# Kernel tuning notes

Hardware: AMD Instinct MI355X
Metric: run time of the kernel (lower is better)

Reference implementation:

```python
import jax, jax.numpy as jnp
import numpy as np

B, T, S = 8, 2048, 512          # batch, visual (tgt) len, audio (src) len
VD, AD, E, H = 512, 256, 512, 8 # v_dim, a_dim, embed_dim, num_heads
D = E // H                      # head_dim = 64
CLAMP = 50000.0


def _xavier(key, fan_in, fan_out):
    limit = float(np.sqrt(6.0 / (fan_in + fan_out)))
    return jax.random.uniform(key, (fan_in, fan_out), jnp.float32, -limit, limit)


def setup_inputs() -> dict:
    key = jax.random.key(0)
    ks = jax.random.split(key, 8)
    return {
        "v": jax.random.normal(ks[0], (B, T, VD), jnp.float32),
        "a": jax.random.normal(ks[1], (B, S, AD), jnp.float32),
        # weights stored [in, out]; biases zero per _reset_parameters
        "w_vq": _xavier(ks[2], VD, E), "b_vq": jnp.zeros((E,), jnp.float32),
        "w_ak": _xavier(ks[3], AD, E), "b_ak": jnp.zeros((E,), jnp.float32),
        "w_vv": _xavier(ks[4], VD, E), "b_vv": jnp.zeros((E,), jnp.float32),
        "w_av": _xavier(ks[5], AD, E), "b_av": jnp.zeros((E,), jnp.float32),
        "w_ov": _xavier(ks[6], E, VD), "b_ov": jnp.zeros((VD,), jnp.float32),
        "w_oa": _xavier(ks[7], E, AD), "b_oa": jnp.zeros((AD,), jnp.float32),
    }


def _heads(x):
    # [B, L, E] -> [B, L, H, D]
    return x.reshape(x.shape[0], x.shape[1], H, D)


def reference(v, a, w_vq, b_vq, w_ak, b_ak, w_vv, b_vv, w_av, b_av,
              w_ov, b_ov, w_oa, b_oa):
    scale = D ** (-0.5)
    q = _heads((v @ w_vq + b_vq) * scale)      # [B,T,H,D]
    k = _heads(a @ w_ak + b_ak)                # [B,S,H,D]
    val_v = _heads(v @ w_vv + b_vv)            # [B,T,H,D]
    val_a = _heads(a @ w_av + b_av)            # [B,S,H,D]

    # shared score matrix [B,H,T,S]
    scores = jnp.einsum('bthd,bshd->bhts', q, k)
    scores = jnp.clip(scores, -CLAMP, CLAMP)

    # audio->visual attention: softmax over last dim of transposed scores
    scores_t = jnp.swapaxes(scores, 2, 3)                     # [B,H,S,T]
    scores_t = scores_t - jnp.max(scores_t, axis=-1, keepdims=True)
    scores_t = jnp.clip(scores_t, -CLAMP, CLAMP)
    attn_a = jax.nn.softmax(scores_t, axis=-1)                # over T

    # visual output attention: softmax over tgt axis (torch dim=1 of [B*H,T,S])
    attn_v = jax.nn.softmax(scores, axis=2)                   # over T

    # dropout is identity in eval mode
    out_v = jnp.einsum('bhts,bshd->bthd', attn_v, val_a).reshape(B, T, E)
    out_a = jnp.einsum('bhst,bthd->bshd', attn_a, val_v).reshape(B, S, E)

    out_v = out_v @ w_ov + b_ov   # [B,T,VD]
    out_a = out_a @ w_oa + b_oa   # [B,S,AD]
    return (out_v, out_a)
```

## Files before the change

kernel.cpp:

```cpp
#include <hip/hip_runtime.h>
#include <hip/hip_bf16.h>
#include <cstdint>

using bf16x8 = __attribute__((ext_vector_type(8))) __bf16;
using bf16x4 = __attribute__((ext_vector_type(4))) __bf16;
using f32x4  = __attribute__((ext_vector_type(4))) float;

constexpr int Bn = 8, Tn = 2048, Sn = 512, VDn = 512, ADn = 256, En = 512, Hn = 8, Dn = 64;

__device__ __forceinline__ f32x4 MFMA(bf16x8 a, bf16x8 b, f32x4 c) {
  return __builtin_amdgcn_mfma_f32_16x16x32_bf16(a, b, c, 0, 0, 0);
}

#define GLOAD_LDS16(gaddr, laddr)                                                     \
  __builtin_amdgcn_global_load_lds(                                                   \
      (const __attribute__((address_space(1))) uint32_t*)(gaddr),                     \
      (__attribute__((address_space(3))) uint32_t*)(laddr), 16, 0, 0)

__global__ __launch_bounds__(256)
void prep_conv_kernel(const float* __restrict__ v, const float* __restrict__ a,
                      __bf16* __restrict__ vbf, __bf16* __restrict__ abf)
{
  constexpr int NV8 = Bn * Tn * VDn / 8;
  const int i = blockIdx.x * 256 + threadIdx.x;
  const float* src; __bf16* dst; size_t off;
  if (i < NV8) { src = v; dst = vbf; off = (size_t)i * 8; }
  else         { src = a; dst = abf; off = (size_t)(i - NV8) * 8; }
  const float4 f0 = *reinterpret_cast<const float4*>(src + off);
  const float4 f1 = *reinterpret_cast<const float4*>(src + off + 4);
  bf16x8 o;
  o[0]=(__bf16)f0.x; o[1]=(__bf16)f0.y; o[2]=(__bf16)f0.z; o[3]=(__bf16)f0.w;
  o[4]=(__bf16)f1.x; o[5]=(__bf16)f1.y; o[6]=(__bf16)f1.z; o[7]=(__bf16)f1.w;
  *reinterpret_cast<bf16x8*>(dst + off) = o;
}

struct TJob { const float* src; __bf16* dst; int K; int N; int tiles; int pad; };
struct TJobs { TJob j[6]; };

__global__ __launch_bounds__(256)
void prep_wt_kernel(TJobs jobs)
{
  __shared__ __bf16 Ts[64][40];
  int b = blockIdx.x;
  int ji = 0;
  while (b >= jobs.j[ji].tiles) { b -= jobs.j[ji].tiles; ++ji; }
  const TJob jb = jobs.j[ji];
  const int tiles_n = jb.N >> 6;
  const int tk = b / tiles_n, tn = b - tk * tiles_n;
  const int t = threadIdx.x;
  {
    const int k = t >> 3, nseg = (t & 7) * 8;
    const float* sp = jb.src + (size_t)(tk * 32 + k) * jb.N + tn * 64 + nseg;
    const float4 f0 = *reinterpret_cast<const float4*>(sp);
    const float4 f1 = *reinterpret_cast<const float4*>(sp + 4);
    Ts[nseg + 0][k] = (__bf16)f0.x; Ts[nseg + 1][k] = (__bf16)f0.y;
    Ts[nseg + 2][k] = (__bf16)f0.z; Ts[nseg + 3][k] = (__bf16)f0.w;
    Ts[nseg + 4][k] = (__bf16)f1.x; Ts[nseg + 5][k] = (__bf16)f1.y;
    Ts[nseg + 6][k] = (__bf16)f1.z; Ts[nseg + 7][k] = (__bf16)f1.w;
  }
  __syncthreads();
  {
    const int n = t >> 2, kk = (t & 3) * 8;
    const bf16x8 vv = *reinterpret_cast<const bf16x8*>(&Ts[n][kk]);
    *reinterpret_cast<bf16x8*>(jb.dst + (size_t)(tn * 64 + n) * jb.K + tk * 32 + kk) = vv;
  }
}

template<int BM_, int OMODE>
__global__ __launch_bounds__(256)
void gemm_bt_kernel(const __bf16* __restrict__ A, const __bf16* __restrict__ WT,
                    const float* __restrict__ bias, void* __restrict__ out,
                    int M, int N, int K, int L, float scale)
{
  constexpr int RI = BM_ / 32;
  constexpr int SEGA = BM_ / 32;
  __shared__ __align__(16) char As[BM_ * 128];
  __shared__ __align__(16) char Ws[128 * 128];
  const int tid = threadIdx.x, lane = tid & 63, w = tid >> 6;
  const int g = lane >> 4, lr = lane & 15;
  const int wr = w >> 1, wc = w & 1;
  const int m0 = blockIdx.y * BM_, n0 = blockIdx.x * 128;

  const int lrow = lane >> 3;
  const int scol = ((lane & 7) << 4) ^ ((lane >> 3) << 4);
  const int fswz = (lr & 7) << 4;

  const char* Ab = (const char*)A;
  const char* Wb = (const char*)WT;

  f32x4 acc[RI][4] = {};

  for (int k0 = 0; k0 < K; k0 += 64) {
    __syncthreads();
    #pragma unroll
    for (int seg = 0; seg < SEGA; ++seg) {
      const int r = w * (SEGA * 8) + seg * 8 + lrow;
      GLOAD_LDS16(Ab + ((size_t)(m0 + r) * K + k0) * 2 + scol, As + (w * SEGA + seg) * 1024);
    }
    #pragma unroll
    for (int seg = 0; seg < 4; ++seg) {
      const int r = w * 32 + seg * 8 + lrow;
      GLOAD_LDS16(Wb + ((size_t)(n0 + r) * K + k0) * 2 + scol, Ws + (w * 4 + seg) * 1024);
    }
    __syncthreads();
    bf16x8 af[RI][2], bf[4][2];
    #pragma unroll
    for (int i = 0; i < RI; ++i)
      #pragma unroll
      for (int kk = 0; kk < 2; ++kk)
        af[i][kk] = *reinterpret_cast<const bf16x8*>(
            As + (wr * (BM_ / 2) + i * 16 + lr) * 128 + ((kk * 64 + g * 16) ^ fswz));
    #pragma unroll
    for (int j = 0; j < 4; ++j)
      #pragma unroll
      for (int kk = 0; kk < 2; ++kk)
        bf[j][kk] = *reinterpret_cast<const bf16x8*>(
            Ws + (wc * 64 + j * 16 + lr) * 128 + ((kk * 64 + g * 16) ^ fswz));
    #pragma unroll
    for (int kk = 0; kk < 2; ++kk)
      #pragma unroll
      for (int i = 0; i < RI; ++i)
        #pragma unroll
        for (int j = 0; j < 4; ++j)
          acc[i][j] = MFMA(af[i][kk], bf[j][kk], acc[i][j]);
  }

  #pragma unroll
  for (int j = 0; j < 4; ++j) {
    const int n = n0 + wc * 64 + j * 16 + lr;
    const float bv = bias[n];
    #pragma unroll
    for (int i = 0; i < RI; ++i) {
      #pragma unroll
      for (int r = 0; r < 4; ++r) {
        const int m = m0 + wr * (BM_ / 2) + i * 16 + g * 4 + r;
        const float val = (acc[i][j][r] + bv) * scale;
        if constexpr (OMODE == 0) {
          const int b = m / L, l = m - b * L;
          const int h = n >> 6, d = n & 63;
          reinterpret_cast<__bf16*>(out)[(((size_t)b * Hn + h) * L + l) * Dn + d] = (__bf16)val;
        } else {
          reinterpret_cast<float*>(out)[(size_t)m * N + n] = val;
        }
      }
    }
  }
}

__global__ __launch_bounds__(512)
void attn_a_kernel(const __bf16* __restrict__ qbf, const __bf16* __restrict__ kbf,
                   const __bf16* __restrict__ vvbf, float* __restrict__ num_ws,
                   float* __restrict__ l_part)
{
  const int bidx = blockIdx.x;
  const int bh = (bidx & 7) + 8 * (bidx >> 6);
  const int rem = (bidx >> 3) & 7;
  const int st = rem & 3, th = rem >> 2;
  const int tid = threadIdx.x, lane = tid & 63, w = tid >> 6;
  const int g = lane >> 4, lr = lane & 15;
  const int s_base = st * 128 + w * 16;

  const char* qp = (const char*)(qbf + ((size_t)bh * Tn + th * 1024) * Dn);
  const __bf16* kp = kbf + (size_t)bh * Sn * Dn;
  const char* vp = (const char*)(vvbf + ((size_t)bh * Tn + th * 1024) * Dn);

  __shared__ __align__(16) char Qs[2][8192];
  __shared__ __align__(16) char VVT[2][8192];
  __shared__ __align__(16) __bf16 Pbuf[8][16][72];

  bf16x8 kf[2];
  #pragma unroll
  for (int dc = 0; dc < 2; ++dc)
    kf[dc] = *reinterpret_cast<const bf16x8*>(kp + (size_t)(s_base + lr) * Dn + dc * 32 + g * 8);

  const int q_src = (w * 8 + (lane >> 3)) * 128 + (((lane & 7) << 4) ^ ((lane >> 3) << 4));
  const int v_src = lane * 128 + (w << 4);
  const int q_swz = (lr & 7) << 4;

  GLOAD_LDS16(qp + q_src, &Qs[0][w * 1024]);
  {
    bf16x8 vreg = *reinterpret_cast<const bf16x8*>(vp + v_src);
    #pragma unroll
    for (int e = 0; e < 8; ++e)
      *(__bf16*)(&VVT[0][(w * 8 + e) * 128 + ((2 * lane) ^ (e << 4))]) = vreg[e];
  }
  __syncthreads();

  f32x4 acc[4] = {};
  float lpart[4] = {};

  for (int ti = 0; ti < 16; ++ti) {
    const int cur = ti & 1, nxt = cur ^ 1;
    const bool more = (ti + 1) < 16;
    bf16x8 vreg_n;
    if (more) {
      GLOAD_LDS16(qp + (size_t)(ti + 1) * 8192 + q_src, &Qs[nxt][w * 1024]);
      vreg_n = *reinterpret_cast<const bf16x8*>(vp + (size_t)(ti + 1) * 8192 + v_src);
    }
    f32x4 sc[4] = {};
    #pragma unroll
    for (int tc = 0; tc < 4; ++tc)
      #pragma unroll
      for (int dc = 0; dc < 2; ++dc) {
        bf16x8 qf = *reinterpret_cast<const bf16x8*>(
            &Qs[cur][(tc * 16 + lr) * 128 + ((dc * 64 + g * 16) ^ q_swz)]);
        sc[tc] = MFMA(kf[dc], qf, sc[tc]);
      }
    #pragma unroll
    for (int tc = 0; tc < 4; ++tc)
      #pragma unroll
      for (int r = 0; r < 4; ++r) {
        const float p = __expf(sc[tc][r]);
        lpart[r] += p;
        Pbuf[w][g * 4 + r][tc * 16 + lr] = (__bf16)p;
      }
    bf16x8 pf[2];
    #pragma unroll
    for (int kc = 0; kc < 2; ++kc)
      pf[kc] = *reinterpret_cast<const bf16x8*>(&Pbuf[w][lr][kc * 32 + g * 8]);
    #pragma unroll
    for (int kc = 0; kc < 2; ++kc)
      #pragma unroll
      for (int j = 0; j < 4; ++j) {
        bf16x8 vf = *reinterpret_cast<const bf16x8*>(
            &VVT[cur][(j * 16 + lr) * 128 + ((kc * 64 + g * 16) ^ q_swz)]);
        acc[j] = MFMA(pf[kc], vf, acc[j]);
      }
    if (more) {
      #pragma unroll
      for (int e = 0; e < 8; ++e)
        *(__bf16*)(&VVT[nxt][(w * 8 + e) * 128 + ((2 * lane) ^ (e << 4))]) = vreg_n[e];
    }
    __syncthreads();
  }

  #pragma unroll
  for (int r = 0; r < 4; ++r) {
    float v = lpart[r];
    v += __shfl_xor(v, 1);
    v += __shfl_xor(v, 2);
    v += __shfl_xor(v, 4);
    v += __shfl_xor(v, 8);
    lpart[r] = v;
  }
  if (lr == 0) {
    #pragma unroll
    for (int r = 0; r < 4; ++r)
      l_part[(size_t)th * 32768 + bh * 512 + s_base + g * 4 + r] = lpart[r];
  }
  float* nump = num_ws + (size_t)th * 2097152 + (size_t)bh * 512 * 64;
  #pragma unroll
  for (int j = 0; j < 4; ++j)
    #pragma unroll
    for (int r = 0; r < 4; ++r)
      nump[(size_t)(s_base + g * 4 + r) * 64 + j * 16 + lr] = acc[j][r];
}

__global__ __launch_bounds__(256)
void combine_kernel(const float* __restrict__ num_ws, const float* __restrict__ l_part,
                    __bf16* __restrict__ oapre, float* __restrict__ l_ws)
{
  const int i = blockIdx.x * 256 + threadIdx.x;
  const int bhs = i >> 4, d4 = i & 15;
  const int bh = bhs >> 9, s = bhs & 511;
  const float lsum = l_part[bhs] + l_part[32768 + bhs];
  const float linv = 1.0f / lsum;
  const f32x4 v0 = *reinterpret_cast<const f32x4*>(num_ws + (size_t)i * 4);
  const f32x4 v1 = *reinterpret_cast<const f32x4*>(num_ws + 2097152 + (size_t)i * 4);
  bf16x4 o;
  #pragma unroll
  for (int e = 0; e < 4; ++e) o[e] = (__bf16)((v0[e] + v1[e]) * linv);
  const int b = bh >> 3, h = bh & 7;
  *reinterpret_cast<bf16x4*>(oapre + ((size_t)(b * 512 + s) * 512 + h * 64 + d4 * 4)) = o;
  if (d4 == 0) l_ws[bhs] = lsum;
}

__global__ __launch_bounds__(256)
void attn_v_kernel(const __bf16* __restrict__ qbf, const __bf16* __restrict__ kbf,
                   const __bf16* __restrict__ vabf, const float* __restrict__ l_ws,
                   __bf16* __restrict__ ovpre)
{
  const int bidx = blockIdx.x;
  const int bh = (bidx & 7) + 8 * (bidx >> 7);
  const int tt = (bidx >> 3) & 15;
  const int b = bh >> 3, h = bh & 7;
  const int tid = threadIdx.x, lane = tid & 63, w = tid >> 6;
  const int g = lane >> 4, lr = lane & 15;
  const int t_base = tt * 128 + w * 32;

  const char* qp = (const char*)(qbf + (size_t)bh * Tn * Dn);
  const char* kp = (const char*)(kbf + (size_t)bh * Sn * Dn);
  const char* vp = (const char*)(vabf + (size_t)bh * Sn * Dn);

  __shared__ __align__(16) char Ks[2][8192];
  __shared__ __align__(16) char VAT[2][8192];
  __shared__ __align__(16) __bf16 Pbuf[4][32][72];
  __shared__ float linv[Sn];

  for (int i = tid; i < Sn; i += 256) linv[i] = 1.0f / l_ws[(size_t)bh * Sn + i];

  bf16x8 qf[2][2];
  #pragma unroll
  for (int tf = 0; tf < 2; ++tf)
    #pragma unroll
    for (int dc = 0; dc < 2; ++dc)
      qf[tf][dc] = *reinterpret_cast<const bf16x8*>(
          qp + ((size_t)(t_base + tf * 16 + lr) * Dn + dc * 32 + g * 8) * 2);

  const int k_src0 = (w * 16 + (lane >> 3)) * 128 + (((lane & 7) << 4) ^ ((lane >> 3) << 4));
  const int v_src = lane * 128 + (w << 5);
  const int swz = (lr & 7) << 4;

  GLOAD_LDS16(kp + k_src0, &Ks[0][w * 2048]);
  GLOAD_LDS16(kp + k_src0 + 1024, &Ks[0][w * 2048 + 1024]);
  {
    bf16x8 va0 = *reinterpret_cast<const bf16x8*>(vp + v_src);
    bf16x8 va1 = *reinterpret_cast<const bf16x8*>(vp + v_src + 16);
    #pragma unroll
    for (int e = 0; e < 8; ++e) {
      *(__bf16*)(&VAT[0][(w * 16 + e) * 128 + ((2 * lane) ^ (e << 4))]) = va0[e];
      *(__bf16*)(&VAT[0][(w * 16 + 8 + e) * 128 + ((2 * lane) ^ (e << 4))]) = va1[e];
    }
  }
  __syncthreads();

  f32x4 acc[2][4] = {};

  for (int si = 0; si < 8; ++si) {
    const int cur = si & 1, nxt = cur ^ 1;
    const bool more = (si + 1) < 8;
    bf16x8 va0n, va1n;
    if (more) {
      GLOAD_LDS16(kp + (size_t)(si + 1) * 8192 + k_src0, &Ks[nxt][w * 2048]);
      GLOAD_LDS16(kp + (size_t)(si + 1) * 8192 + k_src0 + 1024, &Ks[nxt][w * 2048 + 1024]);
      va0n = *reinterpret_cast<const bf16x8*>(vp + (size_t)(si + 1) * 8192 + v_src);
      va1n = *reinterpret_cast<const bf16x8*>(vp + (size_t)(si + 1) * 8192 + v_src + 16);
    }
    f32x4 sc[2][4] = {};
    #pragma unroll
    for (int scn = 0; scn < 4; ++scn)
      #pragma unroll
      for (int dc = 0; dc < 2; ++dc) {
        bf16x8 kfr = *reinterpret_cast<const bf16x8*>(
            &Ks[cur][(scn * 16 + lr) * 128 + ((dc * 64 + g * 16) ^ swz)]);
        #pragma unroll
        for (int tf = 0; tf < 2; ++tf)
          sc[tf][scn] = MFMA(qf[tf][dc], kfr, sc[tf][scn]);
      }
    #pragma unroll
    for (int tf = 0; tf < 2; ++tf)
      #pragma unroll
      for (int scn = 0; scn < 4; ++scn) {
        const float li = linv[si * 64 + scn * 16 + lr];
        #pragma unroll
        for (int r = 0; r < 4; ++r) {
          const float p = __expf(sc[tf][scn][r]) * li;
          Pbuf[w][tf * 16 + g * 4 + r][scn * 16 + lr] = (__bf16)p;
        }
      }
    bf16x8 pf[2][2];
    #pragma unroll
    for (int tf = 0; tf < 2; ++tf)
      #pragma unroll
      for (int kc = 0; kc < 2; ++kc)
        pf[tf][kc] = *reinterpret_cast<const bf16x8*>(&Pbuf[w][tf * 16 + lr][kc * 32 + g * 8]);
    #pragma unroll
    for (int kc = 0; kc < 2; ++kc)
      #pragma unroll
      for (int j = 0; j < 4; ++j) {
        bf16x8 vf = *reinterpret_cast<const bf16x8*>(
            &VAT[cur][(j * 16 + lr) * 128 + ((kc * 64 + g * 16) ^ swz)]);
        #pragma unroll
        for (int tf = 0; tf < 2; ++tf)
          acc[tf][j] = MFMA(pf[tf][kc], vf, acc[tf][j]);
      }
    if (more) {
      #pragma unroll
      for (int e = 0; e < 8; ++e) {
        *(__bf16*)(&VAT[nxt][(w * 16 + e) * 128 + ((2 * lane) ^ (e << 4))]) = va0n[e];
        *(__bf16*)(&VAT[nxt][(w * 16 + 8 + e) * 128 + ((2 * lane) ^ (e << 4))]) = va1n[e];
      }
    }
    __syncthreads();
  }

  #pragma unroll
  for (int tf = 0; tf < 2; ++tf)
    #pragma unroll
    for (int j = 0; j < 4; ++j)
      #pragma unroll
      for (int r = 0; r < 4; ++r)
        ovpre[((size_t)b * Tn + t_base + tf * 16 + g * 4 + r) * En + h * Dn + j * 16 + lr] =
            (__bf16)acc[tf][j][r];
}

extern "C" void kernel_launch(void* const* d_in, const int* in_sizes, int n_in,
                              void* d_out, int out_size, void* d_ws, size_t ws_size,
                              hipStream_t stream)
{
  const float* v    = (const float*)d_in[0];
  const float* a    = (const float*)d_in[1];
  const float* w_vq = (const float*)d_in[2];
  const float* b_vq = (const float*)d_in[3];
  const float* w_ak = (const float*)d_in[4];
  const float* b_ak = (const float*)d_in[5];
  const float* w_vv = (const float*)d_in[6];
  const float* b_vv = (const float*)d_in[7];
  const float* w_av = (const float*)d_in[8];
  const float* b_av = (const float*)d_in[9];
  const float* w_ov = (const float*)d_in[10];
  const float* b_ov = (const float*)d_in[11];
  const float* w_oa = (const float*)d_in[12];
  const float* b_oa = (const float*)d_in[13];

  char* ws = (char*)d_ws;
  __bf16* qbf    = (__bf16*)(ws);
  __bf16* kbf    = (__bf16*)(ws + (16u << 20));
  __bf16* vvbf   = (__bf16*)(ws + (20u << 20));
  __bf16* vabf   = (__bf16*)(ws + (36u << 20));
  __bf16* abf    = (__bf16*)(ws + (40u << 20));
  __bf16* oapre  = (__bf16*)(ws + (40u << 20));
  __bf16* vbf    = (__bf16*)(ws + (44u << 20));
  float*  num_ws = (float*)(ws + (44u << 20));
  __bf16* ovpre  = (__bf16*)(ws + (44u << 20));
  float*  l_part = (float*)(ws + (60u << 20));
  float*  l_ws   = (float*)(ws + (60u << 20) + (256u << 10));
  __bf16* wT     = (__bf16*)(ws + (60u << 20) + (512u << 10));
  __bf16* wTvq = wT;
  __bf16* wTak = wT + 262144;
  __bf16* wTvv = wT + 393216;
  __bf16* wTav = wT + 655360;
  __bf16* wTov = wT + 786432;
  __bf16* wToa = wT + 1048576;

  const float scale_q = 0.125f;

  TJobs jobs;
  jobs.j[0] = { w_vq, wTvq, 512, 512, 128, 0 };
  jobs.j[1] = { w_ak, wTak, 256, 512,  64, 0 };
  jobs.j[2] = { w_vv, wTvv, 512, 512, 128, 0 };
  jobs.j[3] = { w_av, wTav, 256, 512,  64, 0 };
  jobs.j[4] = { w_ov, wTov, 512, 512, 128, 0 };
  jobs.j[5] = { w_oa, wToa, 512, 256,  64, 0 };
  prep_wt_kernel<<<576, 256, 0, stream>>>(jobs);
  prep_conv_kernel<<<4608, 256, 0, stream>>>(v, a, vbf, abf);

  gemm_bt_kernel<128, 0><<<dim3(4, 128), 256, 0, stream>>>(vbf, wTvq, b_vq, qbf,  Bn * Tn, En, VDn, Tn, scale_q);
  gemm_bt_kernel< 64, 0><<<dim3(4,  64), 256, 0, stream>>>(abf, wTak, b_ak, kbf,  Bn * Sn, En, ADn, Sn, 1.0f);
  gemm_bt_kernel<128, 0><<<dim3(4, 128), 256, 0, stream>>>(vbf, wTvv, b_vv, vvbf, Bn * Tn, En, VDn, Tn, 1.0f);
  gemm_bt_kernel< 64, 0><<<dim3(4,  64), 256, 0, stream>>>(abf, wTav, b_av, vabf, Bn * Sn, En, ADn, Sn, 1.0f);

  attn_a_kernel<<<512, 512, 0, stream>>>(qbf, kbf, vvbf, num_ws, l_part);
  combine_kernel<<<2048, 256, 0, stream>>>(num_ws, l_part, oapre, l_ws);
  attn_v_kernel<<<1024, 256, 0, stream>>>(qbf, kbf, vabf, l_ws, ovpre);

  gemm_bt_kernel<128, 1><<<dim3(4, 128), 256, 0, stream>>>(ovpre, wTov, b_ov, (float*)d_out, Bn * Tn, VDn, En, Tn, 1.0f);
  gemm_bt_kernel< 64, 1><<<dim3(2,  64), 256, 0, stream>>>(oapre, wToa, b_oa, (float*)d_out + (size_t)Bn * Tn * VDn, Bn * Sn, ADn, En, Sn, 1.0f);
}
```

Baseline: 262.1 us.

## Fuse paired projection GEMMs and widen attn_v blocks to 512 threads

Merges the Q/V-visual projections into one launch and the K/V-audio projections into another. Each block picks its weight, bias and output pointer based on its N tile, which cuts launch count and lets both halves share the A-operand reads through cache. Block indexing is flattened to 1D with M-tiles as the fast dimension, and the output GEMM is specialized to fp32 output. attn_v_kernel now uses 8 waves of 512 threads covering 256 T rows per block. This halves per-block K/V-audio staging work and redundant loads, at the cost of fewer blocks (512) and more LDS per block.

```diff
diff --git a/kernel.cpp b/kernel.cpp
--- a/kernel.cpp
+++ b/kernel.cpp
@@ -66,20 +66,30 @@
   }
 }
 
-template<int BM_, int OMODE>
+template<int BM_>
 __global__ __launch_bounds__(256)
-void gemm_bt_kernel(const __bf16* __restrict__ A, const __bf16* __restrict__ WT,
-                    const float* __restrict__ bias, void* __restrict__ out,
-                    int M, int N, int K, int L, float scale)
+void gemm_fused_kernel(const __bf16* __restrict__ A,
+                       const __bf16* __restrict__ WT0, const __bf16* __restrict__ WT1,
+                       const float* __restrict__ bias0, const float* __restrict__ bias1,
+                       __bf16* __restrict__ out0, __bf16* __restrict__ out1,
+                       int K, int L, int GY, float scale0)
 {
   constexpr int RI = BM_ / 32;
   constexpr int SEGA = BM_ / 32;
   __shared__ __align__(16) char As[BM_ * 128];
   __shared__ __align__(16) char Ws[128 * 128];
+  const int bid = blockIdx.x;
+  const int by = bid % GY, bx = bid / GY;
   const int tid = threadIdx.x, lane = tid & 63, w = tid >> 6;
   const int g = lane >> 4, lr = lane & 15;
   const int wr = w >> 1, wc = w & 1;
-  const int m0 = blockIdx.y * BM_, n0 = blockIdx.x * 128;
+  const int m0 = by * BM_, n0 = bx * 128;
+
+  const __bf16* WT = (n0 < 512) ? WT0 : WT1;
+  const float* bias = (n0 < 512) ? bias0 : bias1;
+  __bf16* out = (n0 < 512) ? out0 : out1;
+  const float scale = (n0 < 512) ? scale0 : 1.0f;
+  const int nc0 = n0 & 511;
 
   const int lrow = lane >> 3;
   const int scol = ((lane & 7) << 4) ^ ((lane >> 3) << 4);
@@ -100,7 +110,7 @@
     #pragma unroll
     for (int seg = 0; seg < 4; ++seg) {
       const int r = w * 32 + seg * 8 + lrow;
-      GLOAD_LDS16(Wb + ((size_t)(n0 + r) * K + k0) * 2 + scol, Ws + (w * 4 + seg) * 1024);
+      GLOAD_LDS16(Wb + ((size_t)(nc0 + r) * K + k0) * 2 + scol, Ws + (w * 4 + seg) * 1024);
     }
     __syncthreads();
     bf16x8 af[RI][2], bf[4][2];
@@ -127,6 +137,85 @@
 
   #pragma unroll
   for (int j = 0; j < 4; ++j) {
+    const int n = nc0 + wc * 64 + j * 16 + lr;
+    const float bv = bias[n];
+    const int h = n >> 6, d = n & 63;
+    #pragma unroll
+    for (int i = 0; i < RI; ++i) {
+      #pragma unroll
+      for (int r = 0; r < 4; ++r) {
+        const int m = m0 + wr * (BM_ / 2) + i * 16 + g * 4 + r;
+        const int b = m / L, l = m - b * L;
+        const float val = (acc[i][j][r] + bv) * scale;
+        out[(((size_t)b * Hn + h) * L + l) * Dn + d] = (__bf16)val;
+      }
+    }
+  }
+}
+
+template<int BM_>
+__global__ __launch_bounds__(256)
+void gemm_bt_kernel(const __bf16* __restrict__ A, const __bf16* __restrict__ WT,
+                    const float* __restrict__ bias, float* __restrict__ out,
+                    int N, int K, int GY)
+{
+  constexpr int RI = BM_ / 32;
+  constexpr int SEGA = BM_ / 32;
+  __shared__ __align__(16) char As[BM_ * 128];
+  __shared__ __align__(16) char Ws[128 * 128];
+  const int bid = blockIdx.x;
+  const int by = bid % GY, bx = bid / GY;
+  const int tid = threadIdx.x, lane = tid & 63, w = tid >> 6;
+  const int g = lane >> 4, lr = lane & 15;
+  const int wr = w >> 1, wc = w & 1;
+  const int m0 = by * BM_, n0 = bx * 128;
+
+  const int lrow = lane >> 3;
+  const int scol = ((lane & 7) << 4) ^ ((lane >> 3) << 4);
+  const int fswz = (lr & 7) << 4;
+
+  const char* Ab = (const char*)A;
+  const char* Wb = (const char*)WT;
+
+  f32x4 acc[RI][4] = {};
+
+  for (int k0 = 0; k0 < K; k0 += 64) {
+    __syncthreads();
+    #pragma unroll
+    for (int seg = 0; seg < SEGA; ++seg) {
+      const int r = w * (SEGA * 8) + seg * 8 + lrow;
+      GLOAD_LDS16(Ab + ((size_t)(m0 + r) * K + k0) * 2 + scol, As + (w * SEGA + seg) * 1024);
+    }
+    #pragma unroll
+    for (int seg = 0; seg < 4; ++seg) {
+      const int r = w * 32 + seg * 8 + lrow;
+      GLOAD_LDS16(Wb + ((size_t)(n0 + r) * K + k0) * 2 + scol, Ws + (w * 4 + seg) * 1024);
+    }
+    __syncthreads();
+    bf16x8 af[RI][2], bf[4][2];
+    #pragma unroll
+    for (int i = 0; i < RI; ++i)
+      #pragma unroll
+      for (int kk = 0; kk < 2; ++kk)
+        af[i][kk] = *reinterpret_cast<const bf16x8*>(
+            As + (wr * (BM_ / 2) + i * 16 + lr) * 128 + ((kk * 64 + g * 16) ^ fswz));
+    #pragma unroll
+    for (int j = 0; j < 4; ++j)
+      #pragma unroll
+      for (int kk = 0; kk < 2; ++kk)
+        bf[j][kk] = *reinterpret_cast<const bf16x8*>(
+            Ws + (wc * 64 + j * 16 + lr) * 128 + ((kk * 64 + g * 16) ^ fswz));
+    #pragma unroll
+    for (int kk = 0; kk < 2; ++kk)
+      #pragma unroll
+      for (int i = 0; i < RI; ++i)
+        #pragma unroll
+        for (int j = 0; j < 4; ++j)
+          acc[i][j] = MFMA(af[i][kk], bf[j][kk], acc[i][j]);
+  }
+
+  #pragma unroll
+  for (int j = 0; j < 4; ++j) {
     const int n = n0 + wc * 64 + j * 16 + lr;
     const float bv = bias[n];
     #pragma unroll
@@ -134,14 +223,7 @@
       #pragma unroll
       for (int r = 0; r < 4; ++r) {
         const int m = m0 + wr * (BM_ / 2) + i * 16 + g * 4 + r;
-        const float val = (acc[i][j][r] + bv) * scale;
-        if constexpr (OMODE == 0) {
-          const int b = m / L, l = m - b * L;
-          const int h = n >> 6, d = n & 63;
-          reinterpret_cast<__bf16*>(out)[(((size_t)b * Hn + h) * L + l) * Dn + d] = (__bf16)val;
-        } else {
-          reinterpret_cast<float*>(out)[(size_t)m * N + n] = val;
-        }
+        out[(size_t)m * N + n] = acc[i][j][r] + bv;
       }
     }
   }
@@ -275,18 +357,17 @@
   if (d4 == 0) l_ws[bhs] = lsum;
 }
 
-__global__ __launch_bounds__(256)
+__global__ __launch_bounds__(512)
 void attn_v_kernel(const __bf16* __restrict__ qbf, const __bf16* __restrict__ kbf,
                    const __bf16* __restrict__ vabf, const float* __restrict__ l_ws,
                    __bf16* __restrict__ ovpre)
 {
   const int bidx = blockIdx.x;
-  const int bh = (bidx & 7) + 8 * (bidx >> 7);
-  const int tt = (bidx >> 3) & 15;
+  const int bh = bidx & 63, tt = bidx >> 6;
   const int b = bh >> 3, h = bh & 7;
   const int tid = threadIdx.x, lane = tid & 63, w = tid >> 6;
   const int g = lane >> 4, lr = lane & 15;
-  const int t_base = tt * 128 + w * 32;
+  const int t_base = tt * 256 + w * 32;
 
   const char* qp = (const char*)(qbf + (size_t)bh * Tn * Dn);
   const char* kp = (const char*)(kbf + (size_t)bh * Sn * Dn);
@@ -294,10 +375,10 @@
 
   __shared__ __align__(16) char Ks[2][8192];
   __shared__ __align__(16) char VAT[2][8192];
-  __shared__ __align__(16) __bf16 Pbuf[4][32][72];
+  __shared__ __align__(16) __bf16 Pbuf[8][32][72];
   __shared__ float linv[Sn];
 
-  for (int i = tid; i < Sn; i += 256) linv[i] = 1.0f / l_ws[(size_t)bh * Sn + i];
+  if (tid < Sn) linv[tid] = 1.0f / l_ws[(size_t)bh * Sn + tid];
 
   bf16x8 qf[2][2];
   #pragma unroll
@@ -307,20 +388,16 @@
       qf[tf][dc] = *reinterpret_cast<const bf16x8*>(
           qp + ((size_t)(t_base + tf * 16 + lr) * Dn + dc * 32 + g * 8) * 2);
 
-  const int k_src0 = (w * 16 + (lane >> 3)) * 128 + (((lane & 7) << 4) ^ ((lane >> 3) << 4));
-  const int v_src = lane * 128 + (w << 5);
+  const int k_src = (w * 8 + (lane >> 3)) * 128 + (((lane & 7) << 4) ^ ((lane >> 3) << 4));
+  const int v_src = lane * 128 + (w << 4);
   const int swz = (lr & 7) << 4;
 
-  GLOAD_LDS16(kp + k_src0, &Ks[0][w * 2048]);
-  GLOAD_LDS16(kp + k_src0 + 1024, &Ks[0][w * 2048 + 1024]);
+  GLOAD_LDS16(kp + k_src, &Ks[0][w * 1024]);
   {
-    bf16x8 va0 = *reinterpret_cast<const bf16x8*>(vp + v_src);
-    bf16x8 va1 = *reinterpret_cast<const bf16x8*>(vp + v_src + 16);
-    #pragma unroll
-    for (int e = 0; e < 8; ++e) {
-      *(__bf16*)(&VAT[0][(w * 16 + e) * 128 + ((2 * lane) ^ (e << 4))]) = va0[e];
-      *(__bf16*)(&VAT[0][(w * 16 + 8 + e) * 128 + ((2 * lane) ^ (e << 4))]) = va1[e];
-    }
+    bf16x8 va = *reinterpret_cast<const bf16x8*>(vp + v_src);
+    #pragma unroll
+    for (int e = 0; e < 8; ++e)
+      *(__bf16*)(&VAT[0][(w * 8 + e) * 128 + ((2 * lane) ^ (e << 4))]) = va[e];
   }
   __syncthreads();
 
@@ -329,12 +406,10 @@
   for (int si = 0; si < 8; ++si) {
     const int cur = si & 1, nxt = cur ^ 1;
     const bool more = (si + 1) < 8;
-    bf16x8 va0n, va1n;
+    bf16x8 van;
     if (more) {
-      GLOAD_LDS16(kp + (size_t)(si + 1) * 8192 + k_src0, &Ks[nxt][w * 2048]);
-      GLOAD_LDS16(kp + (size_t)(si + 1) * 8192 + k_src0 + 1024, &Ks[nxt][w * 2048 + 1024]);
-      va0n = *reinterpret_cast<const bf16x8*>(vp + (size_t)(si + 1) * 8192 + v_src);
-      va1n = *reinterpret_cast<const bf16x8*>(vp + (size_t)(si + 1) * 8192 + v_src + 16);
+      GLOAD_LDS16(kp + (size_t)(si + 1) * 8192 + k_src, &Ks[nxt][w * 1024]);
+      van = *reinterpret_cast<const bf16x8*>(vp + (size_t)(si + 1) * 8192 + v_src);
     }
     f32x4 sc[2][4] = {};
     #pragma unroll
@@ -376,10 +451,8 @@
       }
     if (more) {
       #pragma unroll
-      for (int e = 0; e < 8; ++e) {
-        *(__bf16*)(&VAT[nxt][(w * 16 + e) * 128 + ((2 * lane) ^ (e << 4))]) = va0n[e];
-        *(__bf16*)(&VAT[nxt][(w * 16 + 8 + e) * 128 + ((2 * lane) ^ (e << 4))]) = va1n[e];
-      }
+      for (int e = 0; e < 8; ++e)
+        *(__bf16*)(&VAT[nxt][(w * 8 + e) * 128 + ((2 * lane) ^ (e << 4))]) = van[e];
     }
     __syncthreads();
   }
@@ -445,15 +518,16 @@
   prep_wt_kernel<<<576, 256, 0, stream>>>(jobs);
   prep_conv_kernel<<<4608, 256, 0, stream>>>(v, a, vbf, abf);
 
-  gemm_bt_kernel<128, 0><<<dim3(4, 128), 256, 0, stream>>>(vbf, wTvq, b_vq, qbf,  Bn * Tn, En, VDn, Tn, scale_q);
-  gemm_bt_kernel< 64, 0><<<dim3(4,  64), 256, 0, stream>>>(abf, wTak, b_ak, kbf,  Bn * Sn, En, ADn, Sn, 1.0f);
-  gemm_bt_kernel<128, 0><<<dim3(4, 128), 256, 0, stream>>>(vbf, wTvv, b_vv, vvbf, Bn * Tn, En, VDn, Tn, 1.0f);
-  gemm_bt_kernel< 64, 0><<<dim3(4,  64), 256, 0, stream>>>(abf, wTav, b_av, vabf, Bn * Sn, En, ADn, Sn, 1.0f);
+  gemm_fused_kernel<128><<<1024, 256, 0, stream>>>(vbf, wTvq, wTvv, b_vq, b_vv,
+                                                   qbf, vvbf, VDn, Tn, 128, scale_q);
+  gemm_fused_kernel< 64><<< 512, 256, 0, stream>>>(abf, wTak, wTav, b_ak, b_av,
+                                                   kbf, vabf, ADn, Sn, 64, 1.0f);
 
   attn_a_kernel<<<512, 512, 0, stream>>>(qbf, kbf, vvbf, num_ws, l_part);
   combine_kernel<<<2048, 256, 0, stream>>>(num_ws, l_part, oapre, l_ws);
-  attn_v_kernel<<<1024, 256, 0, stream>>>(qbf, kbf, vabf, l_ws, ovpre);
-
-  gemm_bt_kernel<128, 1><<<dim3(4, 128), 256, 0, stream>>>(ovpre, wTov, b_ov, (float*)d_out, Bn * Tn, VDn, En, Tn, 1.0f);
-  gemm_bt_kernel< 64, 1><<<dim3(2,  64), 256, 0, stream>>>(oapre, wToa, b_oa, (float*)d_out + (size_t)Bn * Tn * VDn, Bn * Sn, ADn, En, Sn, 1.0f);
-}
+  attn_v_kernel<<<512, 512, 0, stream>>>(qbf, kbf, vabf, l_ws, ovpre);
+
+  gemm_bt_kernel<128><<<512, 256, 0, stream>>>(ovpre, wTov, b_ov, (float*)d_out, VDn, En, 128);
+  gemm_bt_kernel< 64><<<128, 256, 0, stream>>>(oapre, wToa, b_oa,
+                                               (float*)d_out + (size_t)Bn * Tn * VDn, ADn, En, 64);
+}
```

After: 240.7 us. 8.2% less time.
